# Kernel optimization log

Hardware: AMD Instinct MI355X
Metric: run time of the kernel (lower is better)

Reference implementation:

```python
import jax, jax.numpy as jnp
import numpy as np

B, T, I, H, O = 1024, 512, 64, 256, 1

def setup_inputs() -> dict:
    key = jax.random.key(0)
    ks = jax.random.split(key, 12)
    s_ih0 = 1.0 / np.sqrt(H)
    def u(k, shape):
        return jax.random.uniform(k, shape, jnp.float32, -s_ih0, s_ih0)
    return {
        "x": jax.random.normal(ks[0], (B, T, I), jnp.float32),
        "w_ih0": u(ks[1], (4 * H, I)),
        "w_hh0": u(ks[2], (4 * H, H)),
        "b_ih0": u(ks[3], (4 * H,)),
        "b_hh0": u(ks[4], (4 * H,)),
        "w_ih1": u(ks[5], (4 * H, H)),
        "w_hh1": u(ks[6], (4 * H, H)),
        "b_ih1": u(ks[7], (4 * H,)),
        "b_hh1": u(ks[8], (4 * H,)),
        "fc_w": u(ks[9], (O, H)),
        "fc_b": u(ks[10], (O,)),
    }

def _lstm_layer(x, w_ih, w_hh, b_ih, b_hh):
    # x: [B, T, D_in] -> hidden sequence [B, T, H], gate order i,f,g,o (PyTorch)
    b, t, _ = x.shape
    h_dim = w_hh.shape[1]
    # precompute input projections for all timesteps: [T, B, 4H]
    xproj = (jnp.einsum('bti,gi->btg', x, w_ih) + b_ih + b_hh).transpose(1, 0, 2)
    h0 = jnp.zeros((b, h_dim), x.dtype)
    c0 = jnp.zeros((b, h_dim), x.dtype)

    def step(carry, xp):
        h, c = carry
        gates = xp + h @ w_hh.T  # [B, 4H]
        i_g, f_g, g_g, o_g = jnp.split(gates, 4, axis=-1)
        i_g = jax.nn.sigmoid(i_g)
        f_g = jax.nn.sigmoid(f_g)
        g_g = jnp.tanh(g_g)
        o_g = jax.nn.sigmoid(o_g)
        c = f_g * c + i_g * g_g
        h = o_g * jnp.tanh(c)
        return (h, c), h

    (h_last, _), hs = jax.lax.scan(step, (h0, c0), xproj)
    return hs.transpose(1, 0, 2), h_last

def reference(x, w_ih0, w_hh0, b_ih0, b_hh0, w_ih1, w_hh1, b_ih1, b_hh1, fc_w, fc_b):
    # Layer 0 -> (eval mode: dropout is identity) -> Layer 1 -> fc on last step
    h_seq0, _ = _lstm_layer(x, w_ih0, w_hh0, b_ih0, b_hh0)
    _, h_last1 = _lstm_layer(h_seq0, w_ih1, w_hh1, b_ih1, b_hh1)
    return h_last1 @ fc_w.T + fc_b  # [B, O]
```

## Files before the change

### kernel.cpp

```cpp
#include <hip/hip_runtime.h>
#include <stdint.h>


#define T_STEPS 512
#define NC0 10
#define NC1 16
#define WSLICE_ELEMS (4*(NC0+NC1)*512)
#define L1_OFF (4*NC0*512)
#define HN (1024*256)

typedef __attribute__((ext_vector_type(8))) short short8;
typedef __attribute__((ext_vector_type(4))) float floatx4;
typedef _Float16 half8 __attribute__((ext_vector_type(8)));

#define MFMA16(A,B,C) __builtin_amdgcn_mfma_f32_16x16x32_f16( \
    __builtin_bit_cast(half8,(A)), __builtin_bit_cast(half8,(B)), (C), 0, 0, 0)

__device__ __forceinline__ float sigm(float x){
  return __builtin_amdgcn_rcpf(1.0f + __builtin_amdgcn_exp2f(-1.44269504f*x));
}
__device__ __forceinline__ float tanhf_(float x){
  return 1.0f - 2.0f*__builtin_amdgcn_rcpf(1.0f + __builtin_amdgcn_exp2f(2.88539008f*x));
}
__device__ __forceinline__ floatx4 splat4(float v){ return (floatx4){v,v,v,v}; }

__device__ __forceinline__ void cvt8h(const floatx4& v0, const floatx4& v1, short8& hi, short8& lo){
  #pragma unroll
  for (int j = 0; j < 8; ++j){
    float f = (j < 4) ? v0[j] : v1[j-4];
    _Float16 h = (_Float16)f;
    _Float16 l = (_Float16)(f - (float)h);
    hi[j] = (short)__builtin_bit_cast(uint16_t, h);
    lo[j] = (short)__builtin_bit_cast(uint16_t, l);
  }
}

__device__ __forceinline__ short8 load_coh16(const uint16_t* p){
  short8 r;
  asm volatile("global_load_dwordx4 %0, %1, off sc0 sc1" : "=v"(r) : "v"(p));
  return r;
}
__device__ __forceinline__ void store_coh2(uint16_t* p, uint32_t v){
  asm volatile("global_store_short %0, %1, off sc0 sc1" :: "v"(p), "v"(v) : "memory");
}
__device__ __forceinline__ floatx4 load_g16f(const float* p){
  floatx4 r;
  asm volatile("global_load_dwordx4 %0, %1, off" : "=v"(r) : "v"(p));
  return r;
}
#define VM_WAIT(N) do{ asm volatile("s_waitcnt vmcnt(" #N ")" ::: "memory"); \
                       __builtin_amdgcn_sched_barrier(0); }while(0)

__device__ __forceinline__ void arrive(int* c, int lane){
  if (lane == 0)
    __hip_atomic_fetch_add(c, 1, __ATOMIC_RELAXED, __HIP_MEMORY_SCOPE_AGENT);
}
__device__ __forceinline__ void poll_ge(int* c, int target, int lane){
  if (lane == 0){
    int spins = 0;
    int v;
    do {
      v = __hip_atomic_load(c, __ATOMIC_RELAXED, __HIP_MEMORY_SCOPE_AGENT);
      asm volatile("s_waitcnt vmcnt(0)" ::: "memory");
      if (v >= target) break;
      __builtin_amdgcn_s_sleep(1);
    } while (++spins < (1<<20));
  }
  asm volatile("s_waitcnt vmcnt(0)" ::: "memory");
  __builtin_amdgcn_sched_barrier(0);
}

extern "C" __global__ void prep_weights(const float* __restrict__ wih0, const float* __restrict__ whh0,
                                        const float* __restrict__ wih1, const float* __restrict__ whh1,
                                        uint16_t* __restrict__ wfrag)
{
  int idx = blockIdx.x*256 + threadIdx.x;
  int s  = idx / WSLICE_ELEMS;
  int r  = idx - s*WSLICE_ELEMS;
  int layer = (r >= L1_OFF) ? 1 : 0;
  int rr = layer ? (r - L1_OFF) : r;
  int nc = layer ? NC1 : NC0;
  int n  = rr / (nc*512);
  int c  = (rr / 512) % nc;
  int l  = (rr >> 3) & 63;
  int j  = rr & 7;
  int k  = c*32 + ((l >> 4) << 3) + j;
  int grow = n*256 + s*16 + (l & 15);
  float v;
  if (!layer) v = (k < 64)  ? wih0[grow*64  + k] : whh0[grow*256 + (k - 64)];
  else        v = (k < 256) ? wih1[grow*256 + k] : whh1[grow*256 + (k - 256)];
  wfrag[idx] = __builtin_bit_cast(uint16_t, (_Float16)v);
}

extern "C" __global__ void prep_bias(const float* __restrict__ bih0, const float* __restrict__ bhh0,
                                     const float* __restrict__ bih1, const float* __restrict__ bhh1,
                                     float* __restrict__ biasg)
{
  int idx = blockIdx.x*256 + threadIdx.x;
  if (idx >= 16*2*64) return;
  int s = idx >> 7;
  int layer = (idx >> 6) & 1;
  int q = idx & 63;
  int grow = (q >> 4)*256 + s*16 + (q & 15);
  biasg[idx] = layer ? (bih1[grow] + bhh1[grow]) : (bih0[grow] + bhh0[grow]);
}

extern "C" __global__ void __launch_bounds__(256, 1)
lstm_main(const float* __restrict__ x,
          const uint16_t* __restrict__ wfrag,
          const float* __restrict__ biasg,
          uint16_t* __restrict__ hbase,
          const float* __restrict__ fcw,
          const float* __restrict__ fcb,
          int* __restrict__ ctr,
          float* __restrict__ out)
{
  extern __shared__ uint16_t wlds[];
  const int tid  = threadIdx.x;
  const int bid  = blockIdx.x;
  const int s    = bid >> 4;
  const int gh   = bid & 15;
  const int wv   = tid >> 6;
  const int lane = tid & 63;
  const int G    = gh*4 + wv;

  const int arow = G*16 + (lane & 15);
  const int ka   = (lane >> 4) * 8;
  const int drow = G*16 + ((lane >> 4) << 2);
  const int dcol = s*16 + (lane & 15);

  {
    const uint16_t* wsrc = wfrag + (size_t)s*WSLICE_ELEMS;
    for (int i = tid*8; i < WSLICE_ELEMS; i += 256*8)
      *(short8*)(wlds + i) = *(const short8*)(wsrc + i);
  }
  float b0[4], b1[4];
  {
    const int col = lane & 15;
    #pragma unroll
    for (int n = 0; n < 4; ++n){
      b0[n] = biasg[(s*2+0)*64 + n*16 + col];
      b1[n] = biasg[(s*2+1)*64 + n*16 + col];
    }
  }
  const float fcwv = fcw[dcol];
  const float fcb0 = fcb[0];
  __syncthreads();

  const uint16_t* wl = wlds + lane*8;
  const size_t abase = (size_t)arow*256 + ka;
  float c0[4] = {0,0,0,0}, c1[4] = {0,0,0,0};
  int* myc0 = ctr + (G*2+0)*32;
  int* myc1 = ctr + (G*2+1)*32;

  short8 xh[2], xl[2];
  {
    const float* xp = x + (size_t)arow*T_STEPS*64 + ka;
    floatx4 v0 = *(const floatx4*)(xp);
    floatx4 v1 = *(const floatx4*)(xp + 4);
    floatx4 v2 = *(const floatx4*)(xp + 32);
    floatx4 v3 = *(const floatx4*)(xp + 36);
    cvt8h(v0, v1, xh[0], xl[0]);
    cvt8h(v2, v3, xh[1], xl[1]);
  }
  short8 k1h[8], k1l[8];
  {
    const uint16_t* ph = hbase + 4*(size_t)HN + abase;
    const uint16_t* pl = hbase + 6*(size_t)HN + abase;
    #pragma unroll
    for (int kc = 0; kc < 8; ++kc){
      k1h[kc] = load_coh16(ph + kc*32);
      k1l[kc] = load_coh16(pl + kc*32);
    }
    VM_WAIT(0);
  }

  for (int t = 0; t < T_STEPS; ++t){
    const size_t par0  = (size_t)(t & 1);
    const size_t rpar0 = par0 ^ 1;

    poll_ge(myc0, 16*t, lane);

    short8 a0h[8], a0l[8];
    {
      const uint16_t* ph = hbase + rpar0*HN + abase;
      const uint16_t* pl = hbase + 2*(size_t)HN + rpar0*HN + abase;
      #pragma unroll
      for (int kc = 0; kc < 8; ++kc) a0h[kc] = load_coh16(ph + kc*32);
      #pragma unroll
      for (int kc = 0; kc < 8; ++kc) a0l[kc] = load_coh16(pl + kc*32);
    }
    floatx4 xr0, xr1, xr2, xr3;
    {
      const int tn = (t < T_STEPS-1) ? (t+1) : t;
      const float* xp = x + ((size_t)arow*T_STEPS + tn)*64 + ka;
      xr0 = load_g16f(xp);      xr1 = load_g16f(xp + 4);
      xr2 = load_g16f(xp + 32); xr3 = load_g16f(xp + 36);
    }

    floatx4 acc0[4], acc1[4];
    #pragma unroll
    for (int n = 0; n < 4; ++n){ acc0[n] = splat4(b0[n]); acc1[n] = splat4(b1[n]); }
    #pragma unroll
    for (int kc = 0; kc < 8; ++kc){
      #pragma unroll
      for (int n = 0; n < 4; ++n){
        short8 w = *(const short8*)(wl + L1_OFF + (n*NC1 + 8 + kc)*512);
        acc1[n] = MFMA16(k1h[kc], w, acc1[n]);
        acc1[n] = MFMA16(k1l[kc], w, acc1[n]);
      }
    }
    #pragma unroll
    for (int pk = 0; pk < 2; ++pk){
      #pragma unroll
      for (int n = 0; n < 4; ++n){
        short8 w = *(const short8*)(wl + (n*NC0 + pk)*512);
        acc0[n] = MFMA16(xh[pk], w, acc0[n]);
        acc0[n] = MFMA16(xl[pk], w, acc0[n]);
      }
    }

    VM_WAIT(4);

    #pragma unroll
    for (int kc = 0; kc < 8; ++kc){
      #pragma unroll
      for (int n = 0; n < 4; ++n){
        short8 w0 = *(const short8*)(wl + (n*NC0 + 2 + kc)*512);
        acc0[n] = MFMA16(a0h[kc], w0, acc0[n]);
        acc0[n] = MFMA16(a0l[kc], w0, acc0[n]);
        short8 w1 = *(const short8*)(wl + L1_OFF + (n*NC1 + kc)*512);
        acc1[n] = MFMA16(a0h[kc], w1, acc1[n]);
        acc1[n] = MFMA16(a0l[kc], w1, acc1[n]);
      }
    }

    {
      uint16_t* qh = hbase + par0*HN;
      uint16_t* ql = hbase + 2*(size_t)HN + par0*HN;
      #pragma unroll
      for (int r = 0; r < 4; ++r){
        float ig = sigm(acc0[0][r]);
        float fg = sigm(acc0[1][r]);
        float gg = tanhf_(acc0[2][r]);
        float og = sigm(acc0[3][r]);
        c0[r] = fg*c0[r] + ig*gg;
        float h = og*tanhf_(c0[r]);
        _Float16 hh = (_Float16)h;
        _Float16 hl = (_Float16)(h - (float)hh);
        size_t idx = (size_t)(drow + r)*256 + dcol;
        store_coh2(qh + idx, (uint32_t)__builtin_bit_cast(uint16_t, hh));
        store_coh2(ql + idx, (uint32_t)__builtin_bit_cast(uint16_t, hl));
      }
    }
    VM_WAIT(0);
    arrive(myc0, lane);

    cvt8h(xr0, xr1, xh[0], xl[0]);
    cvt8h(xr2, xr3, xh[1], xl[1]);

    if (t > 0){
      uint16_t* qh = hbase + 4*(size_t)HN + rpar0*HN;
      uint16_t* ql = hbase + 6*(size_t)HN + rpar0*HN;
      #pragma unroll
      for (int r = 0; r < 4; ++r){
        float ig = sigm(acc1[0][r]);
        float fg = sigm(acc1[1][r]);
        float gg = tanhf_(acc1[2][r]);
        float og = sigm(acc1[3][r]);
        c1[r] = fg*c1[r] + ig*gg;
        float h = og*tanhf_(c1[r]);
        _Float16 hh = (_Float16)h;
        _Float16 hl = (_Float16)(h - (float)hh);
        size_t idx = (size_t)(drow + r)*256 + dcol;
        store_coh2(qh + idx, (uint32_t)__builtin_bit_cast(uint16_t, hh));
        store_coh2(ql + idx, (uint32_t)__builtin_bit_cast(uint16_t, hl));
      }
    }
    VM_WAIT(0);
    arrive(myc1, lane);

    poll_ge(myc1, 16*(t+1), lane);
    {
      const uint16_t* ph = hbase + 4*(size_t)HN + rpar0*HN + abase;
      const uint16_t* pl = hbase + 6*(size_t)HN + rpar0*HN + abase;
      #pragma unroll
      for (int kc = 0; kc < 8; ++kc){
        k1h[kc] = load_coh16(ph + kc*32);
        k1l[kc] = load_coh16(pl + kc*32);
      }
    }
  }

  {
    const uint16_t* p0h = hbase + 1*(size_t)HN + abase;
    const uint16_t* p0l = hbase + 3*(size_t)HN + abase;
    short8 a0h[8], a0l[8];
    #pragma unroll
    for (int kc = 0; kc < 8; ++kc){
      a0h[kc] = load_coh16(p0h + kc*32);
      a0l[kc] = load_coh16(p0l + kc*32);
    }
    VM_WAIT(0);
    floatx4 acc[4];
    #pragma unroll
    for (int n = 0; n < 4; ++n) acc[n] = splat4(b1[n]);
    #pragma unroll
    for (int kc = 0; kc < 8; ++kc){
      #pragma unroll
      for (int n = 0; n < 4; ++n){
        short8 w1 = *(const short8*)(wl + L1_OFF + (n*NC1 + kc)*512);
        acc[n] = MFMA16(a0h[kc], w1, acc[n]);
        acc[n] = MFMA16(a0l[kc], w1, acc[n]);
        short8 w2 = *(const short8*)(wl + L1_OFF + (n*NC1 + 8 + kc)*512);
        acc[n] = MFMA16(k1h[kc], w2, acc[n]);
        acc[n] = MFMA16(k1l[kc], w2, acc[n]);
      }
    }
    #pragma unroll
    for (int r = 0; r < 4; ++r){
      float ig = sigm(acc[0][r]);
      float fg = sigm(acc[1][r]);
      float gg = tanhf_(acc[2][r]);
      float og = sigm(acc[3][r]);
      float cc = fg*c1[r] + ig*gg;
      float h  = og*tanhf_(cc);
      float v  = h * fcwv;
      v += __shfl_xor(v, 1);
      v += __shfl_xor(v, 2);
      v += __shfl_xor(v, 4);
      v += __shfl_xor(v, 8);
      if ((lane & 15) == 0){
        float res = v + ((s == 0) ? fcb0 : 0.0f);
        atomicAdd(out + drow + r, res);
      }
    }
  }
}

extern "C" void kernel_launch(void* const* d_in, const int* in_sizes, int n_in,
                              void* d_out, int out_size, void* d_ws, size_t ws_size,
                              hipStream_t stream)
{
  (void)in_sizes; (void)n_in; (void)out_size; (void)ws_size;
  const float* x    = (const float*)d_in[0];
  const float* wih0 = (const float*)d_in[1];
  const float* whh0 = (const float*)d_in[2];
  const float* bih0 = (const float*)d_in[3];
  const float* bhh0 = (const float*)d_in[4];
  const float* wih1 = (const float*)d_in[5];
  const float* whh1 = (const float*)d_in[6];
  const float* bih1 = (const float*)d_in[7];
  const float* bhh1 = (const float*)d_in[8];
  const float* fcw  = (const float*)d_in[9];
  const float* fcb  = (const float*)d_in[10];

  char* ws = (char*)d_ws;
  const size_t SZ_WFRAG = (size_t)16*WSLICE_ELEMS*2;
  const size_t OFF_BIAS = SZ_WFRAG;
  const size_t OFF_CTR  = OFF_BIAS + (size_t)16*2*64*4;
  const size_t OFF_H    = (size_t)2*1024*1024;

  uint16_t* wfrag = (uint16_t*)(ws);
  float*    biasg = (float*)(ws + OFF_BIAS);
  int*      ctr   = (int*)(ws + OFF_CTR);
  uint16_t* hbase = (uint16_t*)(ws + OFF_H);
  float*    out   = (float*)d_out;

  hipMemsetAsync(d_out, 0, (size_t)1024*sizeof(float), stream);
  hipMemsetAsync(ws + OFF_CTR, 0, (OFF_H - OFF_CTR) + (size_t)8*HN*2, stream);

  hipLaunchKernelGGL(prep_weights, dim3(16*WSLICE_ELEMS/256), dim3(256), 0, stream,
                     wih0, whh0, wih1, whh1, wfrag);
  hipLaunchKernelGGL(prep_bias, dim3(8), dim3(256), 0, stream,
                     bih0, bhh0, bih1, bhh1, biasg);

  hipFuncSetAttribute((const void*)lstm_main,
                      hipFuncAttributeMaxDynamicSharedMemorySize, WSLICE_ELEMS*2);
  void* args[] = { (void*)&x, (void*)&wfrag, (void*)&biasg, (void*)&hbase,
                   (void*)&fcw, (void*)&fcb, (void*)&ctr, (void*)&out };
  hipError_t ce = hipLaunchCooperativeKernel((void*)lstm_main, dim3(256), dim3(256),
                                             args, WSLICE_ELEMS*2, stream);
  if (ce != hipSuccess){
    hipLaunchKernelGGL(lstm_main, dim3(256), dim3(256), WSLICE_ELEMS*2, stream,
                       x, wfrag, biasg, hbase, fcw, fcb, ctr, out);
  }
}
```

Measured before the change: 5.222 ms.

## Replace per-wave atomic counters with per-block flag arrays polled by vector loads

The cross-block synchronization changes from per-wave atomic fetch-add counters (16 arrivals per group counter) to a per-block flag array. After a __syncthreads, thread 0 of each block stores its step number, and every lane polls all 16 flags of its batch group with four coherent dwordx4 loads, then takes the minimum. This is meant to remove atomic contention and the lane-0 serialized polling. In exchange it adds two block-wide barriers per timestep and has every lane issue redundant polling loads.

```diff
diff --git a/kernel.cpp b/kernel.cpp
--- a/kernel.cpp
+++ b/kernel.cpp
@@ -11,6 +11,7 @@
 
 typedef __attribute__((ext_vector_type(8))) short short8;
 typedef __attribute__((ext_vector_type(4))) float floatx4;
+typedef __attribute__((ext_vector_type(4))) int   intx4;
 typedef _Float16 half8 __attribute__((ext_vector_type(8)));
 
 #define MFMA16(A,B,C) __builtin_amdgcn_mfma_f32_16x16x32_f16( \
@@ -23,6 +24,7 @@
   return 1.0f - 2.0f*__builtin_amdgcn_rcpf(1.0f + __builtin_amdgcn_exp2f(2.88539008f*x));
 }
 __device__ __forceinline__ floatx4 splat4(float v){ return (floatx4){v,v,v,v}; }
+__device__ __forceinline__ int imin2(int a, int b){ return a < b ? a : b; }
 
 __device__ __forceinline__ void cvt8h(const floatx4& v0, const floatx4& v1, short8& hi, short8& lo){
   #pragma unroll
@@ -48,25 +50,33 @@
   asm volatile("global_load_dwordx4 %0, %1, off" : "=v"(r) : "v"(p));
   return r;
 }
+__device__ __forceinline__ void flag_store(int* p, int v){
+  asm volatile("global_store_dword %0, %1, off sc0 sc1" :: "v"(p), "v"(v) : "memory");
+}
+__device__ __forceinline__ intx4 load_flags4(const int* p){
+  intx4 r;
+  asm volatile("global_load_dwordx4 %0, %1, off sc0 sc1" : "=v"(r) : "v"(p));
+  return r;
+}
 #define VM_WAIT(N) do{ asm volatile("s_waitcnt vmcnt(" #N ")" ::: "memory"); \
                        __builtin_amdgcn_sched_barrier(0); }while(0)
 
-__device__ __forceinline__ void arrive(int* c, int lane){
-  if (lane == 0)
-    __hip_atomic_fetch_add(c, 1, __ATOMIC_RELAXED, __HIP_MEMORY_SCOPE_AGENT);
-}
-__device__ __forceinline__ void poll_ge(int* c, int target, int lane){
-  if (lane == 0){
-    int spins = 0;
-    int v;
-    do {
-      v = __hip_atomic_load(c, __ATOMIC_RELAXED, __HIP_MEMORY_SCOPE_AGENT);
-      asm volatile("s_waitcnt vmcnt(0)" ::: "memory");
-      if (v >= target) break;
-      __builtin_amdgcn_s_sleep(1);
-    } while (++spins < (1<<20));
-  }
-  asm volatile("s_waitcnt vmcnt(0)" ::: "memory");
+__device__ __forceinline__ void poll_flags(const int* f, int target){
+  int spins = 0;
+  for(;;){
+    intx4 a = load_flags4(f);
+    intx4 b = load_flags4(f + 4);
+    intx4 c = load_flags4(f + 8);
+    intx4 d = load_flags4(f + 12);
+    VM_WAIT(0);
+    int m = imin2(imin2(a[0],a[1]), imin2(a[2],a[3]));
+    m = imin2(m, imin2(imin2(b[0],b[1]), imin2(b[2],b[3])));
+    m = imin2(m, imin2(imin2(c[0],c[1]), imin2(c[2],c[3])));
+    m = imin2(m, imin2(imin2(d[0],d[1]), imin2(d[2],d[3])));
+    if (m >= target) break;
+    if (++spins > (1<<20)) break;
+    __builtin_amdgcn_s_sleep(1);
+  }
   __builtin_amdgcn_sched_barrier(0);
 }
 
@@ -112,21 +122,20 @@
           uint16_t* __restrict__ hbase,
           const float* __restrict__ fcw,
           const float* __restrict__ fcb,
-          int* __restrict__ ctr,
+          int* __restrict__ flg,
           float* __restrict__ out)
 {
   extern __shared__ uint16_t wlds[];
   const int tid  = threadIdx.x;
   const int bid  = blockIdx.x;
   const int s    = bid >> 4;
-  const int gh   = bid & 15;
+  const int g    = bid & 15;
   const int wv   = tid >> 6;
   const int lane = tid & 63;
-  const int G    = gh*4 + wv;
-
-  const int arow = G*16 + (lane & 15);
+
+  const int arow = g*64 + wv*16 + (lane & 15);
   const int ka   = (lane >> 4) * 8;
-  const int drow = G*16 + ((lane >> 4) << 2);
+  const int drow = g*64 + wv*16 + ((lane >> 4) << 2);
   const int dcol = s*16 + (lane & 15);
 
   {
@@ -150,8 +159,8 @@
   const uint16_t* wl = wlds + lane*8;
   const size_t abase = (size_t)arow*256 + ka;
   float c0[4] = {0,0,0,0}, c1[4] = {0,0,0,0};
-  int* myc0 = ctr + (G*2+0)*32;
-  int* myc1 = ctr + (G*2+1)*32;
+  int* f0 = flg + g*64;
+  int* f1 = flg + 1024 + g*64;
 
   short8 xh[2], xl[2];
   {
@@ -179,7 +188,7 @@
     const size_t par0  = (size_t)(t & 1);
     const size_t rpar0 = par0 ^ 1;
 
-    poll_ge(myc0, 16*t, lane);
+    poll_flags(f0, t);
 
     short8 a0h[8], a0l[8];
     {
@@ -254,7 +263,8 @@
       }
     }
     VM_WAIT(0);
-    arrive(myc0, lane);
+    __syncthreads();
+    if (tid == 0) flag_store(f0 + s, t+1);
 
     cvt8h(xr0, xr1, xh[0], xl[0]);
     cvt8h(xr2, xr3, xh[1], xl[1]);
@@ -278,9 +288,10 @@
       }
     }
     VM_WAIT(0);
-    arrive(myc1, lane);
-
-    poll_ge(myc1, 16*(t+1), lane);
+    __syncthreads();
+    if (tid == 0) flag_store(f1 + s, t+1);
+
+    poll_flags(f1, t+1);
     {
       const uint16_t* ph = hbase + 4*(size_t)HN + rpar0*HN + abase;
       const uint16_t* pl = hbase + 6*(size_t)HN + rpar0*HN + abase;
@@ -358,17 +369,17 @@
   char* ws = (char*)d_ws;
   const size_t SZ_WFRAG = (size_t)16*WSLICE_ELEMS*2;
   const size_t OFF_BIAS = SZ_WFRAG;
-  const size_t OFF_CTR  = OFF_BIAS + (size_t)16*2*64*4;
+  const size_t OFF_FLG  = OFF_BIAS + (size_t)16*2*64*4;
   const size_t OFF_H    = (size_t)2*1024*1024;
 
   uint16_t* wfrag = (uint16_t*)(ws);
   float*    biasg = (float*)(ws + OFF_BIAS);
-  int*      ctr   = (int*)(ws + OFF_CTR);
+  int*      flg   = (int*)(ws + OFF_FLG);
   uint16_t* hbase = (uint16_t*)(ws + OFF_H);
   float*    out   = (float*)d_out;
 
   hipMemsetAsync(d_out, 0, (size_t)1024*sizeof(float), stream);
-  hipMemsetAsync(ws + OFF_CTR, 0, (OFF_H - OFF_CTR) + (size_t)8*HN*2, stream);
+  hipMemsetAsync(ws + OFF_FLG, 0, (OFF_H - OFF_FLG) + (size_t)8*HN*2, stream);
 
   hipLaunchKernelGGL(prep_weights, dim3(16*WSLICE_ELEMS/256), dim3(256), 0, stream,
                      wih0, whh0, wih1, whh1, wfrag);
@@ -378,11 +389,11 @@
   hipFuncSetAttribute((const void*)lstm_main,
                       hipFuncAttributeMaxDynamicSharedMemorySize, WSLICE_ELEMS*2);
   void* args[] = { (void*)&x, (void*)&wfrag, (void*)&biasg, (void*)&hbase,
-                   (void*)&fcw, (void*)&fcb, (void*)&ctr, (void*)&out };
+                   (void*)&fcw, (void*)&fcb, (void*)&flg, (void*)&out };
   hipError_t ce = hipLaunchCooperativeKernel((void*)lstm_main, dim3(256), dim3(256),
                                              args, WSLICE_ELEMS*2, stream);
   if (ce != hipSuccess){
     hipLaunchKernelGGL(lstm_main, dim3(256), dim3(256), WSLICE_ELEMS*2, stream,
-                       x, wfrag, biasg, hbase, fcw, fcb, ctr, out);
-  }
-}
+                       x, wfrag, biasg, hbase, fcw, fcb, flg, out);
+  }
+}
```

Result: faster. 4.971 ms (-4.8%).
